# Optimization experiments

Hardware: AMD Instinct MI355X
Metric: run time of the kernel (lower is better)

The kernel has to match this reference:

```python
import jax, jax.numpy as jnp
import numpy as np

N_NODES = 100000
N_EDGES = 1600000
DIM = 128
N_BUNDLES = 8
BUNDLE_DIM = 4
HIDDEN = 256
TIME = 2


def setup_inputs() -> dict:
    key = jax.random.key(0)
    ks = jax.random.split(key, 8)
    x = jax.random.normal(ks[0], (N_NODES, DIM), dtype=jnp.float32)
    node_rep = jax.random.normal(ks[1], (N_NODES, N_BUNDLES, BUNDLE_DIM, BUNDLE_DIM), dtype=jnp.float32)
    # edge list; ensure every node has out-degree >= 1 so degree norm is finite
    src_extra = jax.random.randint(ks[2], (N_EDGES - N_NODES,), 0, N_NODES)
    src = jnp.concatenate([jnp.arange(N_NODES), src_extra]).astype(jnp.int64)
    dst = jax.random.randint(ks[3], (N_EDGES,), 0, N_NODES).astype(jnp.int64)
    w1 = jax.random.normal(ks[4], (HIDDEN, DIM), dtype=jnp.float32) * (1.0 / np.sqrt(DIM))
    b1 = jnp.zeros((HIDDEN,), dtype=jnp.float32)
    w2 = jax.random.normal(ks[5], (DIM, HIDDEN), dtype=jnp.float32) * (1.0 / np.sqrt(HIDDEN))
    b2 = jnp.zeros((DIM,), dtype=jnp.float32)
    return {"x": x, "node_rep": node_rep, "src": src, "dst": dst,
            "w1": w1, "b1": b1, "w2": w2, "b2": b2}


def reference(x, node_rep, src, dst, w1, b1, w2, b2):
    n = x.shape[0]
    # out-degrees (number of edges with node as source)
    deg = jax.ops.segment_sum(jnp.ones_like(src, dtype=x.dtype), src, num_segments=n)
    # u_mul_v: per-edge product of src and dst degrees -> symmetric norm coefs
    norm_coefs = jax.lax.rsqrt(deg[src] * deg[dst])  # [E]
    # per-bundle rotation: einsum('abcd,abde->abce', node_rep, vf)
    vf = x.reshape(n, N_BUNDLES, BUNDLE_DIM, -1)
    vf = jnp.einsum('nbcd,nbde->nbce', node_rep, vf)
    h = vf.reshape(n, DIM)
    # u_mul_e_sum repeated `time` times: out[dst] += h[src] * coef
    for _ in range(TIME):
        h = jax.ops.segment_sum(h[src] * norm_coefs[:, None], dst, num_segments=n)
    # inverse rotation with transposed node_rep
    vf = h.reshape(n, N_BUNDLES, BUNDLE_DIM, -1)
    vf = jnp.einsum('nbdc,nbde->nbce', node_rep, vf)
    h = vf.reshape(n, DIM)
    # feed-forward (dropout=0, exact GELU as in torch nn.GELU default)
    h = jax.nn.gelu(h @ w1.T + b1, approximate=False)
    return h @ w2.T + b2
```

## Files before the change

### kernel.cpp

```cpp
#include <hip/hip_runtime.h>
#include <hip/hip_bf16.h>
#include <math.h>

#define DIM 128
#define HID 256

typedef short s8x __attribute__((ext_vector_type(8)));
typedef float f4x __attribute__((ext_vector_type(4)));

__device__ __forceinline__ unsigned short f2bf(float f) {
    unsigned int u = __float_as_uint(f);
    u += 0x7FFF + ((u >> 16) & 1);
    return (unsigned short)(u >> 16);
}
__device__ __forceinline__ float bf2f(unsigned short b) {
    return __uint_as_float(((unsigned int)b) << 16);
}
__device__ __forceinline__ float bflo(unsigned int p) {
    return __uint_as_float(p << 16);
}
__device__ __forceinline__ float bfhi(unsigned int p) {
    return __uint_as_float(p & 0xffff0000u);
}


__global__ __launch_bounds__(256) void hist_rot_kernel(
        const int* __restrict__ src, const int* __restrict__ dst,
        int* __restrict__ TD, int* __restrict__ TS, int nE, int nbuck, int chunk,
        int NBE,
        const float* __restrict__ x, const float* __restrict__ R,
        unsigned short* __restrict__ h0,
        const float* __restrict__ w1, const float* __restrict__ w2,
        unsigned short* __restrict__ w1b, unsigned short* __restrict__ w2b,
        int n, int nbRot) {
    __shared__ int hd[1024], hs[1024];
    const int tid = threadIdx.x, blk = blockIdx.x;

    if (blk >= NBE) {
        const int rb = blk - NBE;
        if (rb >= nbRot) {
            int t = (rb - nbRot) * 256 + tid;
            for (int i = t; i < 32768; i += 4096) {
                w1b[i] = f2bf(w1[i]);
                w2b[i] = f2bf(w2[i]);
            }
            return;
        }
        int u = rb * 256 + tid;
        if (u >= n * 8) return;
        int nd = u >> 3, b = u & 7;
        const float* xp = &x[(size_t)nd * DIM + b * 16];
        const float* Rp = &R[(size_t)nd * DIM + b * 16];
        float xv[16], rv[16];
#pragma unroll
        for (int d = 0; d < 4; ++d) {
            *(float4*)&xv[d * 4] = *(const float4*)&xp[d * 4];
            *(float4*)&rv[d * 4] = *(const float4*)&Rp[d * 4];
        }
        unsigned short ob[16];
#pragma unroll
        for (int c = 0; c < 4; ++c)
#pragma unroll
            for (int e = 0; e < 4; ++e) {
                float acc = 0.f;
#pragma unroll
                for (int d = 0; d < 4; ++d) acc += rv[c * 4 + d] * xv[d * 4 + e];
                ob[c * 4 + e] = f2bf(acc);
            }
        unsigned short* op = &h0[(size_t)nd * DIM + b * 16];
        *(s8x*)&op[0] = *(s8x*)&ob[0];
        *(s8x*)&op[8] = *(s8x*)&ob[8];
        return;
    }

    for (int b = tid; b < nbuck; b += 256) { hd[b] = 0; hs[b] = 0; }
    __syncthreads();
    int beg = blk * chunk, end = min(beg + chunk, nE);
    int i = beg + tid;
    for (; i + 256 < end; i += 512) {
        int d0 = dst[i], d1 = dst[i + 256];
        int s0 = src[i], s1 = src[i + 256];
        atomicAdd(&hd[d0 >> 7], 1);
        atomicAdd(&hd[d1 >> 7], 1);
        atomicAdd(&hs[s0 >> 7], 1);
        atomicAdd(&hs[s1 >> 7], 1);
    }
    if (i < end) {
        atomicAdd(&hd[dst[i] >> 7], 1);
        atomicAdd(&hs[src[i] >> 7], 1);
    }
    __syncthreads();
    for (int b = tid; b < nbuck; b += 256) {
        TD[b * NBE + blk] = hd[b];
        TS[b * NBE + blk] = hs[b];
    }
}

__global__ void scan_blocks(const int* in, int* out, int* bsums, int n) {
    __shared__ int part[256];
    const int tid = threadIdx.x;
    const int base = blockIdx.x * 1024 + tid * 4;
    int v[4];
    int sum = 0;
#pragma unroll
    for (int k = 0; k < 4; ++k) {
        v[k] = (base + k < n) ? in[base + k] : 0;
        sum += v[k];
    }
    part[tid] = sum;
    __syncthreads();
    for (int off = 1; off < 256; off <<= 1) {
        int t = (tid >= off) ? part[tid - off] : 0;
        __syncthreads();
        part[tid] += t;
        __syncthreads();
    }
    int excl = part[tid] - sum;
    if (tid == 255) bsums[blockIdx.x] = part[255];
#pragma unroll
    for (int k = 0; k < 4; ++k) {
        if (base + k < n) out[base + k] = excl;
        excl += v[k];
    }
}

__global__ void scan_sums(int* bsums, int nb) {
    __shared__ int part[256];
    const int tid = threadIdx.x;
    const int base = tid * 8;
    int v[8];
    int sum = 0;
#pragma unroll
    for (int k = 0; k < 8; ++k) {
        v[k] = (base + k < nb) ? bsums[base + k] : 0;
        sum += v[k];
    }
    part[tid] = sum;
    __syncthreads();
    for (int off = 1; off < 256; off <<= 1) {
        int t = (tid >= off) ? part[tid - off] : 0;
        __syncthreads();
        part[tid] += t;
        __syncthreads();
    }
    int excl = part[tid] - sum;
#pragma unroll
    for (int k = 0; k < 8; ++k) {
        if (base + k < nb) bsums[base + k] = excl;
        excl += v[k];
    }
}

__global__ void scan_add(int* T, const int* __restrict__ bsums, int n2, int half, int E) {
    int i = blockIdx.x * blockDim.x + threadIdx.x;
    if (i < n2) {
        int v = T[i] + bsums[i >> 10];
        T[i] = (i >= half) ? v - E : v;
    }
}

__global__ __launch_bounds__(256) void scatter_edges(
        const int* __restrict__ src, const int* __restrict__ dst,
        const int* __restrict__ TD, const int* __restrict__ TS,
        unsigned int* __restrict__ pairs, unsigned char* __restrict__ sbyte,
        int nE, int nbuck, int chunk, int NBE) {
    __shared__ int cd[1024], cs[1024];
    const int tid = threadIdx.x, blk = blockIdx.x;
    for (int b = tid; b < nbuck; b += 256) {
        cd[b] = TD[b * NBE + blk];
        cs[b] = TS[b * NBE + blk];
    }
    __syncthreads();
    int beg = blk * chunk, end = min(beg + chunk, nE);
    int i = beg + tid;
    for (; i + 256 < end; i += 512) {
        int s0 = src[i], d0 = dst[i];
        int s1 = src[i + 256], d1 = dst[i + 256];
        int pd0 = atomicAdd(&cd[d0 >> 7], 1);
        pairs[pd0] = ((unsigned)s0 << 7) | (unsigned)(d0 & 127);
        int pd1 = atomicAdd(&cd[d1 >> 7], 1);
        pairs[pd1] = ((unsigned)s1 << 7) | (unsigned)(d1 & 127);
        int ps0 = atomicAdd(&cs[s0 >> 7], 1);
        sbyte[ps0] = (unsigned char)(s0 & 127);
        int ps1 = atomicAdd(&cs[s1 >> 7], 1);
        sbyte[ps1] = (unsigned char)(s1 & 127);
    }
    if (i < end) {
        int s = src[i], d = dst[i];
        int pd = atomicAdd(&cd[d >> 7], 1);
        pairs[pd] = ((unsigned)s << 7) | (unsigned)(d & 127);
        int ps = atomicAdd(&cs[s >> 7], 1);
        sbyte[ps] = (unsigned char)(s & 127);
    }
}

__global__ __launch_bounds__(256) void finalize_src(
        const unsigned char* __restrict__ sbyte, const int* __restrict__ TS,
        float* __restrict__ rdeg, int nE, int nbuck, int nN, int NBE) {
    __shared__ int hist[128];
    const int tid = threadIdx.x, b = blockIdx.x;
    if (tid < 128) hist[tid] = 0;
    __syncthreads();
    int beg = TS[b * NBE];
    int end = (b + 1 < nbuck) ? TS[(b + 1) * NBE] : nE;
    for (int i = beg + tid; i < end; i += 256)
        atomicAdd(&hist[sbyte[i]], 1);
    __syncthreads();
    if (tid < 128) {
        int idx = (b << 7) + tid;
        if (idx < nN) rdeg[idx] = rsqrtf((float)hist[tid]);
    }
}

template<bool PACK>
__global__ __launch_bounds__(256) void finalize_dst(
        const unsigned int* __restrict__ pairs, const int* __restrict__ TD,
        const float* __restrict__ rdeg,
        int* __restrict__ rowstart, uint2* __restrict__ ecsr,
        int* __restrict__ esrcA, int nE, int nbuck, int nN, int NBE) {
    __shared__ int hist[128], sbuf[128], cur[128];
    const int tid = threadIdx.x, b = blockIdx.x;
    int beg = TD[b * NBE];
    int end = (b + 1 < nbuck) ? TD[(b + 1) * NBE] : nE;
    if (tid < 128) hist[tid] = 0;
    __syncthreads();
    for (int i = beg + tid; i < end; i += 256)
        atomicAdd(&hist[(int)(pairs[i] & 127u)], 1);
    __syncthreads();
    int v = (tid < 128) ? hist[tid] : 0;
    if (tid < 128) sbuf[tid] = v;
    __syncthreads();
    for (int off = 1; off < 128; off <<= 1) {
        int t = (tid < 128 && tid >= off) ? sbuf[tid - off] : 0;
        __syncthreads();
        if (tid < 128) sbuf[tid] += t;
        __syncthreads();
    }
    if (tid < 128) {
        int excl = sbuf[tid] - v;
        cur[tid] = excl;
        int idx = (b << 7) + tid;
        if (idx <= nN) rowstart[idx] = beg + excl;
    }
    __syncthreads();
    for (int i = beg + tid; i < end; i += 256) {
        unsigned int p = pairs[i];
        int l = (int)(p & 127u);
        int s = (int)(p >> 7);
        int pos = atomicAdd(&cur[l], 1);
        if (PACK) {
            float coef = rdeg[s] * rdeg[(b << 7) + l];
            ecsr[beg + pos] = make_uint2((unsigned)s, __float_as_uint(coef));
        } else {
            esrcA[beg + pos] = s;
        }
    }
}

template<bool PACK, bool ROT>
__global__ __launch_bounds__(256) void gather_kernel(
        const unsigned short* __restrict__ hsrc,
        const uint2* __restrict__ ecsr, const int* __restrict__ esrcA,
        const float* __restrict__ rdeg, const int* __restrict__ rowstart,
        const float* __restrict__ R,
        unsigned short* __restrict__ hdst, int n) {
    const int node = blockIdx.x * 16 + (threadIdx.x >> 4);
    const int lane = threadIdx.x & 15;
    if (node >= n) return;
    const int beg = rowstart[node];
    const int end = rowstart[node + 1];
    float rd = 0.f;
    if (!PACK) rd = rdeg[node];

    float4 r0, r1;
    if (ROT) {
        r0 = *(const float4*)&R[(size_t)node * DIM + lane * 8];
        r1 = *(const float4*)&R[(size_t)node * DIM + lane * 8 + 4];
    }

    float a0 = 0.f, a1 = 0.f, a2 = 0.f, a3 = 0.f;
    float a4 = 0.f, a5 = 0.f, a6 = 0.f, a7 = 0.f;
    int i = beg;
    for (; i + 8 <= end; i += 8) {
        int s0, s1, s2, s3, s4, s5, s6, s7;
        float c0, c1, c2, c3, c4, c5, c6, c7;
        if (PACK) {
            uint2 e0 = ecsr[i],     e1 = ecsr[i + 1], e2 = ecsr[i + 2], e3 = ecsr[i + 3];
            uint2 e4 = ecsr[i + 4], e5 = ecsr[i + 5], e6 = ecsr[i + 6], e7 = ecsr[i + 7];
            s0 = (int)e0.x; c0 = __uint_as_float(e0.y);
            s1 = (int)e1.x; c1 = __uint_as_float(e1.y);
            s2 = (int)e2.x; c2 = __uint_as_float(e2.y);
            s3 = (int)e3.x; c3 = __uint_as_float(e3.y);
            s4 = (int)e4.x; c4 = __uint_as_float(e4.y);
            s5 = (int)e5.x; c5 = __uint_as_float(e5.y);
            s6 = (int)e6.x; c6 = __uint_as_float(e6.y);
            s7 = (int)e7.x; c7 = __uint_as_float(e7.y);
        } else {
            s0 = esrcA[i];     s1 = esrcA[i + 1]; s2 = esrcA[i + 2]; s3 = esrcA[i + 3];
            s4 = esrcA[i + 4]; s5 = esrcA[i + 5]; s6 = esrcA[i + 6]; s7 = esrcA[i + 7];
            c0 = rdeg[s0] * rd; c1 = rdeg[s1] * rd;
            c2 = rdeg[s2] * rd; c3 = rdeg[s3] * rd;
            c4 = rdeg[s4] * rd; c5 = rdeg[s5] * rd;
            c6 = rdeg[s6] * rd; c7 = rdeg[s7] * rd;
        }
        uint4 p0 = *(const uint4*)&hsrc[(size_t)s0 * DIM + lane * 8];
        uint4 p1 = *(const uint4*)&hsrc[(size_t)s1 * DIM + lane * 8];
        uint4 p2 = *(const uint4*)&hsrc[(size_t)s2 * DIM + lane * 8];
        uint4 p3 = *(const uint4*)&hsrc[(size_t)s3 * DIM + lane * 8];
        uint4 p4 = *(const uint4*)&hsrc[(size_t)s4 * DIM + lane * 8];
        uint4 p5 = *(const uint4*)&hsrc[(size_t)s5 * DIM + lane * 8];
        uint4 p6 = *(const uint4*)&hsrc[(size_t)s6 * DIM + lane * 8];
        uint4 p7 = *(const uint4*)&hsrc[(size_t)s7 * DIM + lane * 8];
        a0 += bflo(p0.x) * c0 + bflo(p1.x) * c1 + bflo(p2.x) * c2 + bflo(p3.x) * c3
            + bflo(p4.x) * c4 + bflo(p5.x) * c5 + bflo(p6.x) * c6 + bflo(p7.x) * c7;
        a1 += bfhi(p0.x) * c0 + bfhi(p1.x) * c1 + bfhi(p2.x) * c2 + bfhi(p3.x) * c3
            + bfhi(p4.x) * c4 + bfhi(p5.x) * c5 + bfhi(p6.x) * c6 + bfhi(p7.x) * c7;
        a2 += bflo(p0.y) * c0 + bflo(p1.y) * c1 + bflo(p2.y) * c2 + bflo(p3.y) * c3
            + bflo(p4.y) * c4 + bflo(p5.y) * c5 + bflo(p6.y) * c6 + bflo(p7.y) * c7;
        a3 += bfhi(p0.y) * c0 + bfhi(p1.y) * c1 + bfhi(p2.y) * c2 + bfhi(p3.y) * c3
            + bfhi(p4.y) * c4 + bfhi(p5.y) * c5 + bfhi(p6.y) * c6 + bfhi(p7.y) * c7;
        a4 += bflo(p0.z) * c0 + bflo(p1.z) * c1 + bflo(p2.z) * c2 + bflo(p3.z) * c3
            + bflo(p4.z) * c4 + bflo(p5.z) * c5 + bflo(p6.z) * c6 + bflo(p7.z) * c7;
        a5 += bfhi(p0.z) * c0 + bfhi(p1.z) * c1 + bfhi(p2.z) * c2 + bfhi(p3.z) * c3
            + bfhi(p4.z) * c4 + bfhi(p5.z) * c5 + bfhi(p6.z) * c6 + bfhi(p7.z) * c7;
        a6 += bflo(p0.w) * c0 + bflo(p1.w) * c1 + bflo(p2.w) * c2 + bflo(p3.w) * c3
            + bflo(p4.w) * c4 + bflo(p5.w) * c5 + bflo(p6.w) * c6 + bflo(p7.w) * c7;
        a7 += bfhi(p0.w) * c0 + bfhi(p1.w) * c1 + bfhi(p2.w) * c2 + bfhi(p3.w) * c3
            + bfhi(p4.w) * c4 + bfhi(p5.w) * c5 + bfhi(p6.w) * c6 + bfhi(p7.w) * c7;
    }
    for (; i + 4 <= end; i += 4) {
        int s0, s1, s2, s3;
        float c0, c1, c2, c3;
        if (PACK) {
            uint2 e0 = ecsr[i], e1 = ecsr[i + 1], e2 = ecsr[i + 2], e3 = ecsr[i + 3];
            s0 = (int)e0.x; c0 = __uint_as_float(e0.y);
            s1 = (int)e1.x; c1 = __uint_as_float(e1.y);
            s2 = (int)e2.x; c2 = __uint_as_float(e2.y);
            s3 = (int)e3.x; c3 = __uint_as_float(e3.y);
        } else {
            s0 = esrcA[i]; s1 = esrcA[i + 1]; s2 = esrcA[i + 2]; s3 = esrcA[i + 3];
            c0 = rdeg[s0] * rd; c1 = rdeg[s1] * rd;
            c2 = rdeg[s2] * rd; c3 = rdeg[s3] * rd;
        }
        uint4 p0 = *(const uint4*)&hsrc[(size_t)s0 * DIM + lane * 8];
        uint4 p1 = *(const uint4*)&hsrc[(size_t)s1 * DIM + lane * 8];
        uint4 p2 = *(const uint4*)&hsrc[(size_t)s2 * DIM + lane * 8];
        uint4 p3 = *(const uint4*)&hsrc[(size_t)s3 * DIM + lane * 8];
        a0 += bflo(p0.x) * c0 + bflo(p1.x) * c1 + bflo(p2.x) * c2 + bflo(p3.x) * c3;
        a1 += bfhi(p0.x) * c0 + bfhi(p1.x) * c1 + bfhi(p2.x) * c2 + bfhi(p3.x) * c3;
        a2 += bflo(p0.y) * c0 + bflo(p1.y) * c1 + bflo(p2.y) * c2 + bflo(p3.y) * c3;
        a3 += bfhi(p0.y) * c0 + bfhi(p1.y) * c1 + bfhi(p2.y) * c2 + bfhi(p3.y) * c3;
        a4 += bflo(p0.z) * c0 + bflo(p1.z) * c1 + bflo(p2.z) * c2 + bflo(p3.z) * c3;
        a5 += bfhi(p0.z) * c0 + bfhi(p1.z) * c1 + bfhi(p2.z) * c2 + bfhi(p3.z) * c3;
        a6 += bflo(p0.w) * c0 + bflo(p1.w) * c1 + bflo(p2.w) * c2 + bflo(p3.w) * c3;
        a7 += bfhi(p0.w) * c0 + bfhi(p1.w) * c1 + bfhi(p2.w) * c2 + bfhi(p3.w) * c3;
    }
    for (; i < end; ++i) {
        int s0;
        float c0;
        if (PACK) {
            uint2 e0 = ecsr[i];
            s0 = (int)e0.x; c0 = __uint_as_float(e0.y);
        } else {
            s0 = esrcA[i];
            c0 = rdeg[s0] * rd;
        }
        uint4 p0 = *(const uint4*)&hsrc[(size_t)s0 * DIM + lane * 8];
        a0 += bflo(p0.x) * c0;
        a1 += bfhi(p0.x) * c0;
        a2 += bflo(p0.y) * c0;
        a3 += bfhi(p0.y) * c0;
        a4 += bflo(p0.z) * c0;
        a5 += bfhi(p0.z) * c0;
        a6 += bflo(p0.w) * c0;
        a7 += bfhi(p0.w) * c0;
    }

    unsigned short ob[8];
    if (ROT) {
        const int half = lane & 1;
        float av[8] = {a0, a1, a2, a3, a4, a5, a6, a7};
        float rown[8] = {r0.x, r0.y, r0.z, r0.w, r1.x, r1.y, r1.z, r1.w};
        float hb[16], rv[16];
#pragma unroll
        for (int j = 0; j < 8; ++j) {
            float ho = __shfl_xor(av[j], 1);
            float ro = __shfl_xor(rown[j], 1);
            hb[j]     = half ? ho      : av[j];
            hb[8 + j] = half ? av[j]   : ho;
            rv[j]     = half ? ro      : rown[j];
            rv[8 + j] = half ? rown[j] : ro;
        }
        float rr[2][4];
#pragma unroll
        for (int cc = 0; cc < 2; ++cc)
#pragma unroll
            for (int d = 0; d < 4; ++d)
                rr[cc][d] = half ? rv[d * 4 + 2 + cc] : rv[d * 4 + cc];
#pragma unroll
        for (int cc = 0; cc < 2; ++cc)
#pragma unroll
            for (int e = 0; e < 4; ++e) {
                float acc = 0.f;
#pragma unroll
                for (int d = 0; d < 4; ++d) acc += rr[cc][d] * hb[d * 4 + e];
                ob[cc * 4 + e] = f2bf(acc);
            }
    } else {
        ob[0] = f2bf(a0); ob[1] = f2bf(a1); ob[2] = f2bf(a2); ob[3] = f2bf(a3);
        ob[4] = f2bf(a4); ob[5] = f2bf(a5); ob[6] = f2bf(a6); ob[7] = f2bf(a7);
    }
    uint4 o;
    o.x = (unsigned)ob[0] | ((unsigned)ob[1] << 16);
    o.y = (unsigned)ob[2] | ((unsigned)ob[3] << 16);
    o.z = (unsigned)ob[4] | ((unsigned)ob[5] << 16);
    o.w = (unsigned)ob[6] | ((unsigned)ob[7] << 16);
    *(uint4*)&hdst[(size_t)node * DIM + lane * 8] = o;
}

#define HBST 264
__global__ __launch_bounds__(256, 4) void ffn_kernel(
        const unsigned short* __restrict__ h,
        const unsigned short* __restrict__ w1b,
        const float* __restrict__ b1,
        const unsigned short* __restrict__ w2b,
        const float* __restrict__ b2,
        float* __restrict__ out, int n) {
    __shared__ unsigned short hbuf[64 * HBST];
    const int tid  = threadIdx.x;
    const int node0 = blockIdx.x * 64;
    const int wave = tid >> 6;
    const int lane = tid & 63;
    const int lr = lane & 15;
    const int lq = lane >> 4;

    const unsigned short* hbase = &h[(size_t)node0 * DIM];

    f4x acc1[4][4];
#pragma unroll
    for (int mt = 0; mt < 4; ++mt)
#pragma unroll
        for (int nt = 0; nt < 4; ++nt) acc1[mt][nt] = (f4x){0.f, 0.f, 0.f, 0.f};

    const int nw = wave * 64;
#pragma unroll
    for (int ks = 0; ks < 4; ++ks) {
        const int k0 = ks * 32 + lq * 8;
        s8x af[4], bfv[4];
#pragma unroll
        for (int mt = 0; mt < 4; ++mt)
            af[mt] = *(const s8x*)&hbase[(size_t)(mt * 16 + lr) * DIM + k0];
#pragma unroll
        for (int nt = 0; nt < 4; ++nt)
            bfv[nt] = *(const s8x*)&w1b[(size_t)(nw + nt * 16 + lr) * 128 + k0];
#pragma unroll
        for (int mt = 0; mt < 4; ++mt)
#pragma unroll
            for (int nt = 0; nt < 4; ++nt)
                acc1[mt][nt] = __builtin_amdgcn_mfma_f32_16x16x32_bf16(
                    af[mt], bfv[nt], acc1[mt][nt], 0, 0, 0);
    }

#pragma unroll
    for (int nt = 0; nt < 4; ++nt) {
        int nn = nw + nt * 16 + lr;
        float bias = b1[nn];
#pragma unroll
        for (int mt = 0; mt < 4; ++mt) {
#pragma unroll
            for (int r = 0; r < 4; ++r) {
                float v = acc1[mt][nt][r] + bias;
                v = 0.5f * v * (1.f + erff(v * 0.70710678118654752f));
                hbuf[(mt * 16 + lq * 4 + r) * HBST + nn] = f2bf(v);
            }
        }
    }
    __syncthreads();

    f4x acc2[4][2];
#pragma unroll
    for (int mt = 0; mt < 4; ++mt)
#pragma unroll
        for (int nt = 0; nt < 2; ++nt) acc2[mt][nt] = (f4x){0.f, 0.f, 0.f, 0.f};

    const int nw2 = wave * 32;
#pragma unroll
    for (int ks = 0; ks < 8; ++ks) {
        const int k0 = ks * 32 + lq * 8;
        s8x af[4], bf2v[2];
#pragma unroll
        for (int mt = 0; mt < 4; ++mt)
            af[mt] = *(const s8x*)&hbuf[(mt * 16 + lr) * HBST + k0];
#pragma unroll
        for (int nt = 0; nt < 2; ++nt)
            bf2v[nt] = *(const s8x*)&w2b[(size_t)(nw2 + nt * 16 + lr) * 256 + k0];
#pragma unroll
        for (int mt = 0; mt < 4; ++mt)
#pragma unroll
            for (int nt = 0; nt < 2; ++nt)
                acc2[mt][nt] = __builtin_amdgcn_mfma_f32_16x16x32_bf16(
                    af[mt], bf2v[nt], acc2[mt][nt], 0, 0, 0);
    }
#pragma unroll
    for (int nt = 0; nt < 2; ++nt) {
        int n2 = nw2 + nt * 16 + lr;
        float bias = b2[n2];
#pragma unroll
        for (int mt = 0; mt < 4; ++mt) {
#pragma unroll
            for (int r = 0; r < 4; ++r) {
                int gn = node0 + mt * 16 + lq * 4 + r;
                if (gn < n) out[(size_t)gn * DIM + n2] = acc2[mt][nt][r] + bias;
            }
        }
    }
}

extern "C" void kernel_launch(void* const* d_in, const int* in_sizes, int n_in,
                              void* d_out, int out_size, void* d_ws, size_t ws_size,
                              hipStream_t stream) {
    const float* x   = (const float*)d_in[0];
    const float* R   = (const float*)d_in[1];
    const int*   src = (const int*)d_in[2];
    const int*   dst = (const int*)d_in[3];
    const float* w1  = (const float*)d_in[4];
    const float* b1  = (const float*)d_in[5];
    const float* w2  = (const float*)d_in[6];
    const float* b2  = (const float*)d_in[7];
    float* out = (float*)d_out;

    const int N = in_sizes[0] / DIM;
    const int E = in_sizes[2];

    const int nbuck = (N + 127) >> 7;
    const int NBE = 256;
    const int chunk = (E + NBE - 1) / NBE;
    const int nScan = nbuck * NBE;
    const int nScan2 = 2 * nScan;
    const int nbScan2 = (nScan2 + 1023) / 1024;

    unsigned short* hA = (unsigned short*)d_ws;
    unsigned short* hM = hA + (size_t)N * DIM;
    unsigned int*  pairs = (unsigned int*)hM;
    unsigned char* sbyte = (unsigned char*)(pairs + E);
    char* edge_base = (char*)(hM + (size_t)N * DIM);

    const size_t tail_bytes = (size_t)N * 4 + (size_t)(N + 1) * 4 +
                              (size_t)nScan * 8 + 2048 * 4 + (size_t)2 * 32768 * 2;
    const size_t fixed_bytes = (size_t)N * DIM * 4;
    const bool use_pack = (fixed_bytes + (size_t)E * 8 + tail_bytes) <= ws_size;
    const size_t edge_bytes = use_pack ? (size_t)E * 8 : (size_t)E * 4;

    uint2* ecsr  = (uint2*)edge_base;
    int*   esrcA = (int*)edge_base;
    char* q = edge_base + edge_bytes;
    float* rdeg     = (float*)q;
    int*   rowstart = (int*)(rdeg + N);
    int*   TD       = rowstart + (N + 1);
    int*   TS       = TD + nScan;
    int*   bsums    = TS + nScan;
    unsigned short* w1b = (unsigned short*)(bsums + 2048);
    unsigned short* w2b = w1b + 32768;

    const int BLK = 256;

    const int nbRot = ((size_t)N * 8 + BLK - 1) / BLK;
    hist_rot_kernel<<<NBE + nbRot + 16, BLK, 0, stream>>>(
        src, dst, TD, TS, E, nbuck, chunk, NBE,
        x, R, hA, w1, w2, w1b, w2b, N, nbRot);

    scan_blocks<<<nbScan2, BLK, 0, stream>>>(TD, TD, bsums, nScan2);
    scan_sums<<<1, BLK, 0, stream>>>(bsums, nbScan2);
    scan_add<<<(nScan2 + BLK - 1) / BLK, BLK, 0, stream>>>(TD, bsums, nScan2, nScan, E);
    scatter_edges<<<NBE, BLK, 0, stream>>>(src, dst, TD, TS, pairs, sbyte, E, nbuck, chunk, NBE);
    finalize_src<<<nbuck, BLK, 0, stream>>>(sbyte, TS, rdeg, E, nbuck, N, NBE);
    if (use_pack)
        finalize_dst<true><<<nbuck, BLK, 0, stream>>>(pairs, TD, rdeg, rowstart,
                                                      ecsr, esrcA, E, nbuck, N, NBE);
    else
        finalize_dst<false><<<nbuck, BLK, 0, stream>>>(pairs, TD, rdeg, rowstart,
                                                       ecsr, esrcA, E, nbuck, N, NBE);

    const int nbG = (N + 15) / 16;
    if (use_pack) {
        gather_kernel<true , false><<<nbG, BLK, 0, stream>>>(hA, ecsr, esrcA, rdeg,
                                                             rowstart, R, hM, N);
        gather_kernel<true , true ><<<nbG, BLK, 0, stream>>>(hM, ecsr, esrcA, rdeg,
                                                             rowstart, R, hA, N);
    } else {
        gather_kernel<false, false><<<nbG, BLK, 0, stream>>>(hA, ecsr, esrcA, rdeg,
                                                             rowstart, R, hM, N);
        gather_kernel<false, true ><<<nbG, BLK, 0, stream>>>(hM, ecsr, esrcA, rdeg,
                                                             rowstart, R, hA, N);
    }

    ffn_kernel<<<(N + 63) / 64, BLK, 0, stream>>>(hA, w1b, b1, w2b, b2, out, N);
}
```

Measured before the change: 416.8 us.

## Sort destination nodes by in-degree to balance gather work across wavefronts

Builds a per-bucket in-degree histogram in finalize_dst, scans it, and scatters node ids into a degree-sorted permutation. The gather kernels then process nodes in that order, so the 16-lane groups sharing a wavefront have similar edge counts and divergence is reduced. The 8-wide unrolled edge loop is also dropped, leaving the 4-wide loop. This adds four extra launches plus an indirection through perm, and output writes now land in permuted rather than contiguous order.

```diff
diff --git a/kernel.cpp b/kernel.cpp
--- a/kernel.cpp
+++ b/kernel.cpp
@@ -217,18 +217,24 @@
         const unsigned int* __restrict__ pairs, const int* __restrict__ TD,
         const float* __restrict__ rdeg,
         int* __restrict__ rowstart, uint2* __restrict__ ecsr,
-        int* __restrict__ esrcA, int nE, int nbuck, int nN, int NBE) {
-    __shared__ int hist[128], sbuf[128], cur[128];
+        int* __restrict__ esrcA, int* __restrict__ TP,
+        int nE, int nbuck, int nN, int NBE) {
+    __shared__ int hist[128], sbuf[128], cur[128], hist2[512];
     const int tid = threadIdx.x, b = blockIdx.x;
     int beg = TD[b * NBE];
     int end = (b + 1 < nbuck) ? TD[(b + 1) * NBE] : nE;
     if (tid < 128) hist[tid] = 0;
+    for (int t = tid; t < 512; t += 256) hist2[t] = 0;
     __syncthreads();
     for (int i = beg + tid; i < end; i += 256)
         atomicAdd(&hist[(int)(pairs[i] & 127u)], 1);
     __syncthreads();
     int v = (tid < 128) ? hist[tid] : 0;
-    if (tid < 128) sbuf[tid] = v;
+    if (tid < 128) {
+        sbuf[tid] = v;
+        int idx = (b << 7) + tid;
+        if (idx < nN) atomicAdd(&hist2[min(v, 511)], 1);
+    }
     __syncthreads();
     for (int off = 1; off < 128; off <<= 1) {
         int t = (tid < 128 && tid >= off) ? sbuf[tid - off] : 0;
@@ -242,6 +248,7 @@
         int idx = (b << 7) + tid;
         if (idx <= nN) rowstart[idx] = beg + excl;
     }
+    for (int t = tid; t < 512; t += 256) TP[t * nbuck + b] = hist2[t];
     __syncthreads();
     for (int i = beg + tid; i < end; i += 256) {
         unsigned int p = pairs[i];
@@ -257,16 +264,35 @@
     }
 }
 
+__global__ __launch_bounds__(256) void perm_scatter(
+        const int* __restrict__ rowstart, const int* __restrict__ TP,
+        int* __restrict__ perm, int nbuck, int nN) {
+    __shared__ int cur[512];
+    const int tid = threadIdx.x, b = blockIdx.x;
+    for (int t = tid; t < 512; t += 256) cur[t] = TP[t * nbuck + b];
+    __syncthreads();
+    if (tid < 128) {
+        int v = (b << 7) + tid;
+        if (v < nN) {
+            int deg = rowstart[v + 1] - rowstart[v];
+            int bin = min(deg, 511);
+            int pos = atomicAdd(&cur[bin], 1);
+            perm[pos] = v;
+        }
+    }
+}
+
 template<bool PACK, bool ROT>
 __global__ __launch_bounds__(256) void gather_kernel(
         const unsigned short* __restrict__ hsrc,
         const uint2* __restrict__ ecsr, const int* __restrict__ esrcA,
         const float* __restrict__ rdeg, const int* __restrict__ rowstart,
-        const float* __restrict__ R,
+        const float* __restrict__ R, const int* __restrict__ perm,
         unsigned short* __restrict__ hdst, int n) {
-    const int node = blockIdx.x * 16 + (threadIdx.x >> 4);
+    const int gi = blockIdx.x * 16 + (threadIdx.x >> 4);
     const int lane = threadIdx.x & 15;
-    if (node >= n) return;
+    if (gi >= n) return;
+    const int node = perm[gi];
     const int beg = rowstart[node];
     const int end = rowstart[node + 1];
     float rd = 0.f;
@@ -281,53 +307,6 @@
     float a0 = 0.f, a1 = 0.f, a2 = 0.f, a3 = 0.f;
     float a4 = 0.f, a5 = 0.f, a6 = 0.f, a7 = 0.f;
     int i = beg;
-    for (; i + 8 <= end; i += 8) {
-        int s0, s1, s2, s3, s4, s5, s6, s7;
-        float c0, c1, c2, c3, c4, c5, c6, c7;
-        if (PACK) {
-            uint2 e0 = ecsr[i],     e1 = ecsr[i + 1], e2 = ecsr[i + 2], e3 = ecsr[i + 3];
-            uint2 e4 = ecsr[i + 4], e5 = ecsr[i + 5], e6 = ecsr[i + 6], e7 = ecsr[i + 7];
-            s0 = (int)e0.x; c0 = __uint_as_float(e0.y);
-            s1 = (int)e1.x; c1 = __uint_as_float(e1.y);
-            s2 = (int)e2.x; c2 = __uint_as_float(e2.y);
-            s3 = (int)e3.x; c3 = __uint_as_float(e3.y);
-            s4 = (int)e4.x; c4 = __uint_as_float(e4.y);
-            s5 = (int)e5.x; c5 = __uint_as_float(e5.y);
-            s6 = (int)e6.x; c6 = __uint_as_float(e6.y);
-            s7 = (int)e7.x; c7 = __uint_as_float(e7.y);
-        } else {
-            s0 = esrcA[i];     s1 = esrcA[i + 1]; s2 = esrcA[i + 2]; s3 = esrcA[i + 3];
-            s4 = esrcA[i + 4]; s5 = esrcA[i + 5]; s6 = esrcA[i + 6]; s7 = esrcA[i + 7];
-            c0 = rdeg[s0] * rd; c1 = rdeg[s1] * rd;
-            c2 = rdeg[s2] * rd; c3 = rdeg[s3] * rd;
-            c4 = rdeg[s4] * rd; c5 = rdeg[s5] * rd;
-            c6 = rdeg[s6] * rd; c7 = rdeg[s7] * rd;
-        }
-        uint4 p0 = *(const uint4*)&hsrc[(size_t)s0 * DIM + lane * 8];
-        uint4 p1 = *(const uint4*)&hsrc[(size_t)s1 * DIM + lane * 8];
-        uint4 p2 = *(const uint4*)&hsrc[(size_t)s2 * DIM + lane * 8];
-        uint4 p3 = *(const uint4*)&hsrc[(size_t)s3 * DIM + lane * 8];
-        uint4 p4 = *(const uint4*)&hsrc[(size_t)s4 * DIM + lane * 8];
-        uint4 p5 = *(const uint4*)&hsrc[(size_t)s5 * DIM + lane * 8];
-        uint4 p6 = *(const uint4*)&hsrc[(size_t)s6 * DIM + lane * 8];
-        uint4 p7 = *(const uint4*)&hsrc[(size_t)s7 * DIM + lane * 8];
-        a0 += bflo(p0.x) * c0 + bflo(p1.x) * c1 + bflo(p2.x) * c2 + bflo(p3.x) * c3
-            + bflo(p4.x) * c4 + bflo(p5.x) * c5 + bflo(p6.x) * c6 + bflo(p7.x) * c7;
-        a1 += bfhi(p0.x) * c0 + bfhi(p1.x) * c1 + bfhi(p2.x) * c2 + bfhi(p3.x) * c3
-            + bfhi(p4.x) * c4 + bfhi(p5.x) * c5 + bfhi(p6.x) * c6 + bfhi(p7.x) * c7;
-        a2 += bflo(p0.y) * c0 + bflo(p1.y) * c1 + bflo(p2.y) * c2 + bflo(p3.y) * c3
-            + bflo(p4.y) * c4 + bflo(p5.y) * c5 + bflo(p6.y) * c6 + bflo(p7.y) * c7;
-        a3 += bfhi(p0.y) * c0 + bfhi(p1.y) * c1 + bfhi(p2.y) * c2 + bfhi(p3.y) * c3
-            + bfhi(p4.y) * c4 + bfhi(p5.y) * c5 + bfhi(p6.y) * c6 + bfhi(p7.y) * c7;
-        a4 += bflo(p0.z) * c0 + bflo(p1.z) * c1 + bflo(p2.z) * c2 + bflo(p3.z) * c3
-            + bflo(p4.z) * c4 + bflo(p5.z) * c5 + bflo(p6.z) * c6 + bflo(p7.z) * c7;
-        a5 += bfhi(p0.z) * c0 + bfhi(p1.z) * c1 + bfhi(p2.z) * c2 + bfhi(p3.z) * c3
-            + bfhi(p4.z) * c4 + bfhi(p5.z) * c5 + bfhi(p6.z) * c6 + bfhi(p7.z) * c7;
-        a6 += bflo(p0.w) * c0 + bflo(p1.w) * c1 + bflo(p2.w) * c2 + bflo(p3.w) * c3
-            + bflo(p4.w) * c4 + bflo(p5.w) * c5 + bflo(p6.w) * c6 + bflo(p7.w) * c7;
-        a7 += bfhi(p0.w) * c0 + bfhi(p1.w) * c1 + bfhi(p2.w) * c2 + bfhi(p3.w) * c3
-            + bfhi(p4.w) * c4 + bfhi(p5.w) * c5 + bfhi(p6.w) * c6 + bfhi(p7.w) * c7;
-    }
     for (; i + 4 <= end; i += 4) {
         int s0, s1, s2, s3;
         float c0, c1, c2, c3;
@@ -538,6 +517,8 @@
     const int nScan = nbuck * NBE;
     const int nScan2 = 2 * nScan;
     const int nbScan2 = (nScan2 + 1023) / 1024;
+    const int nP = 512 * nbuck;
+    const int nbScanP = (nP + 1023) / 1024;
 
     unsigned short* hA = (unsigned short*)d_ws;
     unsigned short* hM = hA + (size_t)N * DIM;
@@ -546,7 +527,9 @@
     char* edge_base = (char*)(hM + (size_t)N * DIM);
 
     const size_t tail_bytes = (size_t)N * 4 + (size_t)(N + 1) * 4 +
-                              (size_t)nScan * 8 + 2048 * 4 + (size_t)2 * 32768 * 2;
+                              (size_t)nScan * 8 + 2048 * 4 +
+                              (size_t)nP * 4 + (size_t)N * 4 +
+                              (size_t)2 * 32768 * 2;
     const size_t fixed_bytes = (size_t)N * DIM * 4;
     const bool use_pack = (fixed_bytes + (size_t)E * 8 + tail_bytes) <= ws_size;
     const size_t edge_bytes = use_pack ? (size_t)E * 8 : (size_t)E * 4;
@@ -559,7 +542,9 @@
     int*   TD       = rowstart + (N + 1);
     int*   TS       = TD + nScan;
     int*   bsums    = TS + nScan;
-    unsigned short* w1b = (unsigned short*)(bsums + 2048);
+    int*   TP       = bsums + 2048;
+    int*   perm     = TP + nP;
+    unsigned short* w1b = (unsigned short*)(perm + N);
     unsigned short* w2b = w1b + 32768;
 
     const int BLK = 256;
@@ -576,22 +561,27 @@
     finalize_src<<<nbuck, BLK, 0, stream>>>(sbyte, TS, rdeg, E, nbuck, N, NBE);
     if (use_pack)
         finalize_dst<true><<<nbuck, BLK, 0, stream>>>(pairs, TD, rdeg, rowstart,
-                                                      ecsr, esrcA, E, nbuck, N, NBE);
+                                                      ecsr, esrcA, TP, E, nbuck, N, NBE);
     else
         finalize_dst<false><<<nbuck, BLK, 0, stream>>>(pairs, TD, rdeg, rowstart,
-                                                       ecsr, esrcA, E, nbuck, N, NBE);
+                                                       ecsr, esrcA, TP, E, nbuck, N, NBE);
+
+    scan_blocks<<<nbScanP, BLK, 0, stream>>>(TP, TP, bsums, nP);
+    scan_sums<<<1, BLK, 0, stream>>>(bsums, nbScanP);
+    scan_add<<<(nP + BLK - 1) / BLK, BLK, 0, stream>>>(TP, bsums, nP, nP, 0);
+    perm_scatter<<<nbuck, BLK, 0, stream>>>(rowstart, TP, perm, nbuck, N);
 
     const int nbG = (N + 15) / 16;
     if (use_pack) {
         gather_kernel<true , false><<<nbG, BLK, 0, stream>>>(hA, ecsr, esrcA, rdeg,
-                                                             rowstart, R, hM, N);
+                                                             rowstart, R, perm, hM, N);
         gather_kernel<true , true ><<<nbG, BLK, 0, stream>>>(hM, ecsr, esrcA, rdeg,
-                                                             rowstart, R, hA, N);
+                                                             rowstart, R, perm, hA, N);
     } else {
         gather_kernel<false, false><<<nbG, BLK, 0, stream>>>(hA, ecsr, esrcA, rdeg,
-                                                             rowstart, R, hM, N);
+                                                             rowstart, R, perm, hM, N);
         gather_kernel<false, true ><<<nbG, BLK, 0, stream>>>(hM, ecsr, esrcA, rdeg,
-                                                             rowstart, R, hA, N);
+                                                             rowstart, R, perm, hA, N);
     }
 
     ffn_kernel<<<(N + 63) / 64, BLK, 0, stream>>>(hA, w1b, b1, w2b, b2, out, N);
```

Measured after the change: 436.0 us. 1.05x slower.
